# Kernel tuning notes

Measured on AMD Instinct MI355X. Metric: run time of the kernel, lower is better.

The kernel has to match this reference:

```python
import jax, jax.numpy as jnp
import numpy as np
from jax import lax

C = 512          # in_channels
L = 4            # fcos_conv_layers
NUM_CLS = 1      # fcos_num_class - 1
PRIOR_BIAS = float(-np.log((1 - 0.01) / 0.01))
BN_EPS = 1e-5


def conv1d(x, w, b, pad):
    # x: [B, Cin, T], w: [Cout, Cin, K]
    y = lax.conv_general_dilated(x, w, window_strides=(1,), padding=[(pad, pad)],
                                 dimension_numbers=('NCH', 'OIH', 'NCH'))
    return y + b[None, :, None]


def bn(x, g, b, m, v):
    inv = lax.rsqrt(v + BN_EPS)
    return (x - m[None, :, None]) * (g * inv)[None, :, None] + b[None, :, None]


def tower(x, ws, bs, gs, bes, ms, vs):
    # ws: [L, C, C, 3]; fixed small loop over layers
    for i in range(L):
        x = jax.nn.relu(bn(conv1d(x, ws[i], bs[i], 1), gs[i], bes[i], ms[i], vs[i]))
    return x


def setup_inputs() -> dict:
    key = jax.random.key(0)
    ks = jax.random.split(key, 32)
    d = {}
    d['f0'] = jax.random.normal(ks[0], (8, C, 1024), jnp.float32)
    d['f1'] = jax.random.normal(ks[1], (8, C, 512), jnp.float32)
    d['f2'] = jax.random.normal(ks[2], (8, C, 256), jnp.float32)

    def nrm(k, shape):
        return 0.01 * jax.random.normal(k, shape, jnp.float32)

    # cls / bbox towers: stacked conv + BN params
    d['cls_tw_w'] = nrm(ks[3], (L, C, C, 3)); d['cls_tw_b'] = jnp.zeros((L, C))
    d['cls_bn_g'] = jnp.ones((L, C)); d['cls_bn_b'] = jnp.zeros((L, C))
    d['cls_bn_m'] = jnp.zeros((L, C)); d['cls_bn_v'] = jnp.ones((L, C))
    d['box_tw_w'] = nrm(ks[4], (L, C, C, 3)); d['box_tw_b'] = jnp.zeros((L, C))
    d['box_bn_g'] = jnp.ones((L, C)); d['box_bn_b'] = jnp.zeros((L, C))
    d['box_bn_m'] = jnp.zeros((L, C)); d['box_bn_v'] = jnp.ones((L, C))

    d['logits_w'] = nrm(ks[5], (NUM_CLS, C, 3))
    d['logits_b'] = jnp.full((NUM_CLS,), PRIOR_BIAS, jnp.float32)
    d['bbox_w'] = nrm(ks[6], (2, C, 3)); d['bbox_b'] = jnp.zeros((2,))

    d['mix_w'] = nrm(ks[7], (C, 2 * C, 1)); d['mix_b'] = jnp.zeros((C,))
    d['mix_bn_g'] = jnp.ones((C,)); d['mix_bn_b'] = jnp.zeros((C,))
    d['mix_bn_m'] = jnp.zeros((C,)); d['mix_bn_v'] = jnp.ones((C,))

    d['iou_w1'] = nrm(ks[8], (C // 2, C, 3)); d['iou_b1'] = jnp.zeros((C // 2,))
    d['iou_bn_g'] = jnp.ones((C // 2,)); d['iou_bn_b'] = jnp.zeros((C // 2,))
    d['iou_bn_m'] = jnp.zeros((C // 2,)); d['iou_bn_v'] = jnp.ones((C // 2,))
    d['iou_w2'] = nrm(ks[9], (1, C // 2, 1)); d['iou_b2'] = jnp.zeros((1,))

    d['scales'] = jnp.ones((3,), jnp.float32)
    return d


def reference(f0, f1, f2,
              cls_tw_w, cls_tw_b, cls_bn_g, cls_bn_b, cls_bn_m, cls_bn_v,
              box_tw_w, box_tw_b, box_bn_g, box_bn_b, box_bn_m, box_bn_v,
              logits_w, logits_b, bbox_w, bbox_b,
              mix_w, mix_b, mix_bn_g, mix_bn_b, mix_bn_m, mix_bn_v,
              iou_w1, iou_b1, iou_bn_g, iou_bn_b, iou_bn_m, iou_bn_v,
              iou_w2, iou_b2, scales):
    outs = []
    for l, x in enumerate([f0, f1, f2]):
        ct = tower(x, cls_tw_w, cls_tw_b, cls_bn_g, cls_bn_b, cls_bn_m, cls_bn_v)
        bt = tower(x, box_tw_w, box_tw_b, box_bn_g, box_bn_b, box_bn_m, box_bn_v)
        logits = conv1d(ct, logits_w, logits_b, 1)                      # [B, 1, T]
        bbox = jnp.exp(conv1d(bt, bbox_w, bbox_b, 1) * scales[l])       # [B, 2, T]
        mix = jax.nn.relu(bn(conv1d(jnp.concatenate([ct, bt], axis=1), mix_w, mix_b, 0),
                             mix_bn_g, mix_bn_b, mix_bn_m, mix_bn_v))   # [B, C, T]
        h = jax.nn.relu(bn(conv1d(mix, iou_w1, iou_b1, 1),
                           iou_bn_g, iou_bn_b, iou_bn_m, iou_bn_v))
        iou = conv1d(h, iou_w2, iou_b2, 0)                              # [B, 1, T]
        outs.append(jnp.concatenate([logits, bbox, iou], axis=1))       # [B, 4, T]
    return jnp.concatenate(outs, axis=-1)  # [B, 4, T0+T1+T2]
```

## Files before the change

kernel.cpp:

```cpp
#include <hip/hip_runtime.h>
#include <hip/hip_bf16.h>


typedef __bf16 bf16x8 __attribute__((ext_vector_type(8)));
typedef float f32x4 __attribute__((ext_vector_type(4)));

__device__ __forceinline__ float bf2f(unsigned short u) {
    union { unsigned int i; float f; } c; c.i = ((unsigned int)u) << 16; return c.f;
}
__device__ __forceinline__ unsigned short f2bf(float f) {
    union { __hip_bfloat16 h; unsigned short u; } c; c.h = __float2bfloat16(f); return c.u;
}

__device__ __forceinline__ void gload16(const void* g, void* l) {
    __builtin_amdgcn_global_load_lds(
        (const __attribute__((address_space(1))) unsigned int*)g,
        (__attribute__((address_space(3))) unsigned int*)l,
        16, 0, 0);
}

__device__ __forceinline__ void tile_decode(int ct, int& rowstart, int& t0, int& Tl) {
    if (ct < 64)      { Tl = 1024; int b = ct >> 3;                 t0 = (ct & 7) << 7; rowstart = b * 1026 + 1; }
    else if (ct < 96) { Tl = 512;  int i = ct - 64; int b = i >> 2; t0 = (i & 3) << 7; rowstart = 8208 + b * 514 + 1; }
    else              { Tl = 256;  int i = ct - 96; int b = i >> 1; t0 = (i & 1) << 7; rowstart = 12320 + b * 258 + 1; }
}

__global__ __launch_bounds__(256, 2)
void conv_tower(const unsigned short* __restrict__ X, int xstride, int ci_twstride,
                const unsigned short* __restrict__ W,
                const float* __restrict__ Bs,
                unsigned short* __restrict__ Y)
{
    __shared__ alignas(16) unsigned short Xb[2][9 * 512];
    __shared__ alignas(16) unsigned short Wb[3][16 * 512];
    constexpr int XBSZ = 9 * 512;
    constexpr int WBSZ = 16 * 512;
    constexpr int XBYTES = XBSZ * 2;
    constexpr int WBYTES = WBSZ * 2;

    const int L = blockIdx.x;
    const int P = (L & 7) * 56 + (L >> 3);
    const int ct = P >> 2, sub = P & 3;
    const int tw = sub >> 1, co0 = (sub & 1) << 8;

    int rowstart, t0, Tl;
    tile_decode(ct, rowstart, t0, Tl);
    const int rtile = rowstart + t0;

    const int tid = threadIdx.x, lane = tid & 63, wid = tid >> 6;
    const int wco = (wid >> 1) << 7;
    const int wt  = (wid & 1) << 6;
    const int lr = lane & 15, sr = lane >> 4;

    const unsigned short* Wp = W + (size_t)tw * 3145728;
    const float* Bp = Bs + tw * 2048;
    const int co_out0 = tw * 512 + co0;
    const int ci_off = tw * ci_twstride;

    const unsigned short* xga[3]; unsigned short* xl[3];
#pragma unroll
    for (int p = 0; p < 3; ++p) {
        int seg = (p < 2) ? (p * 4 + wid) : 8;
        xl[p] = (unsigned short*)Xb[0] + seg * 512;
        int row = seg * 16 + (lane >> 2);
        int sc = (lane & 3) ^ ((row >> 1) & 3);
        xga[p] = X + (size_t)(rtile - 1 + row) * xstride + ci_off + sc * 8;
    }
    const unsigned short* wga[4]; unsigned short* wl[4];
#pragma unroll
    for (int p = 0; p < 4; ++p) {
        int seg = p * 4 + wid;
        wl[p] = (unsigned short*)Wb[0] + seg * 512;
        int row = seg * 16 + (lane >> 2);
        int sc = (lane & 3) ^ ((row >> 1) & 3);
        wga[p] = Wp + (size_t)(co0 + row) * 1536 + sc * 8;
    }

    int aoff[8];
#pragma unroll
    for (int mi = 0; mi < 8; ++mi) {
        int ra = wco + mi * 16 + lr;
        aoff[mi] = ra * 64 + (((sr ^ (ra >> 1)) & 3) << 4);
    }
    int boff[3][4];
#pragma unroll
    for (int kk = 0; kk < 3; ++kk)
#pragma unroll
        for (int ni = 0; ni < 4; ++ni) {
            int rb = wt + ni * 16 + lr + kk;
            boff[kk][ni] = rb * 64 + (((sr ^ (rb >> 1)) & 3) << 4);
        }

    f32x4 acc[8][4];
#pragma unroll
    for (int i = 0; i < 8; ++i)
#pragma unroll
        for (int j = 0; j < 4; ++j) acc[i][j] = (f32x4){0.f, 0.f, 0.f, 0.f};

#pragma unroll
    for (int p = 0; p < 3; ++p) gload16(xga[p], xl[p]);
#pragma unroll
    for (int p = 0; p < 4; ++p) {
        gload16(wga[p],       wl[p]);
        gload16(wga[p] + 512, wl[p] + WBSZ);
    }
    asm volatile("s_waitcnt vmcnt(0)" ::: "memory");
    __builtin_amdgcn_s_barrier();

#pragma unroll
    for (int s = 0; s < 48; ++s) {
        const int kk = s % 3, k0 = s / 3;
        if      (s == 47) asm volatile("s_waitcnt vmcnt(0)" ::: "memory");
        else if (s == 46) asm volatile("s_waitcnt vmcnt(4)" ::: "memory");
        else if (kk == 0) asm volatile("s_waitcnt vmcnt(4)" ::: "memory");
        else              asm volatile("s_waitcnt vmcnt(7)" ::: "memory");
        __builtin_amdgcn_s_barrier();

        if (s + 2 <= 47) {
            const int u = s + 2, ut = u % 3, uk = u / 3;
#pragma unroll
            for (int p = 0; p < 4; ++p)
                gload16(wga[p] + ut * 512 + uk * 32, wl[p] + ut * WBSZ);
        }
        if (kk == 0 && k0 + 1 <= 15) {
#pragma unroll
            for (int p = 0; p < 3; ++p)
                gload16(xga[p] + (k0 + 1) * 32, xl[p] + ((k0 + 1) & 1) * XBSZ);
        }

        const char* wbuf = (const char*)Wb[0] + (s % 3) * WBYTES;
        const char* xbuf = (const char*)Xb[0] + (k0 & 1) * XBYTES;
        bf16x8 af[8], bv[4];
#pragma unroll
        for (int mi = 0; mi < 8; ++mi)
            af[mi] = *(const bf16x8*)(wbuf + aoff[mi]);
#pragma unroll
        for (int ni = 0; ni < 4; ++ni)
            bv[ni] = *(const bf16x8*)(xbuf + boff[kk][ni]);
        __builtin_amdgcn_s_setprio(1);
#pragma unroll
        for (int mi = 0; mi < 8; ++mi)
#pragma unroll
            for (int ni = 0; ni < 4; ++ni)
                acc[mi][ni] = __builtin_amdgcn_mfma_f32_16x16x32_bf16(af[mi], bv[ni], acc[mi][ni], 0, 0, 0);
        __builtin_amdgcn_s_setprio(0);
        __builtin_amdgcn_s_barrier();
    }

    const int r4 = sr * 4;
#pragma unroll
    for (int mi = 0; mi < 8; ++mi) {
        int co_l = wco + mi * 16 + r4;
        float b0 = Bp[co0 + co_l + 0], b1 = Bp[co0 + co_l + 1];
        float b2 = Bp[co0 + co_l + 2], b3 = Bp[co0 + co_l + 3];
#pragma unroll
        for (int ni = 0; ni < 4; ++ni) {
            int t = wt + ni * 16 + lr;
            f32x4 a = acc[mi][ni];
            float v0 = fmaxf(a[0] + b0, 0.f), v1 = fmaxf(a[1] + b1, 0.f);
            float v2 = fmaxf(a[2] + b2, 0.f), v3 = fmaxf(a[3] + b3, 0.f);
            union { unsigned long long u; unsigned short s[4]; } pk2;
            pk2.s[0] = f2bf(v0); pk2.s[1] = f2bf(v1); pk2.s[2] = f2bf(v2); pk2.s[3] = f2bf(v3);
            *(unsigned long long*)(Y + (size_t)(rtile + t) * 1024 + co_out0 + co_l) = pk2.u;
        }
    }
}

template<int KSIZE>
__global__ __launch_bounds__(256)
void conv_gemm(const unsigned short* __restrict__ X, int xstride, int ci0_base, int ci_twstride, int Cin,
               const unsigned short* __restrict__ W, int w_twstride,
               const float* __restrict__ Bs, int b_twstride,
               unsigned short* __restrict__ Y, int ystride, int co_twstride,
               int relu)
{
    constexpr int BM = 128, BN = 128, BK = 32;
    constexpr int NR = BN + KSIZE - 1;
    constexpr int XSEG = (NR * 64 + 1023) / 1024;
    constexpr int XPW  = (XSEG + 3) / 4;
    constexpr int WSEG = KSIZE * BM * 64 / 1024;
    constexpr int WPW  = WSEG / 4;
    __shared__ alignas(16) unsigned short Xs[2 * XSEG * 512];
    __shared__ alignas(16) unsigned short Ws[2 * WSEG * 512];

    const int tid = threadIdx.x;
    const int lane = tid & 63, wid = tid >> 6;
    int rowstart, t0, Tl;
    tile_decode(blockIdx.x, rowstart, t0, Tl);
    const int co0 = blockIdx.y * BM;
    const int tw = blockIdx.z;
    const int ci_off = ci0_base + tw * ci_twstride;
    const unsigned short* Wp = W + (size_t)tw * w_twstride;
    const float* Bp = Bs + tw * b_twstride;
    const int co_out0 = tw * co_twstride + co0;

    const int wm = (wid >> 1) * 64, wn = (wid & 1) * 64;
    const int lr = lane & 15;
    const int sr = lane >> 4;

    const unsigned short* xga[XPW]; unsigned short* xl[XPW];
#pragma unroll
    for (int p = 0; p < XPW; ++p) {
        int seg = (KSIZE == 3) ? ((p < 2) ? p * 4 + wid : 8) : (p * 4 + wid);
        xl[p] = Xs + seg * 512;
        int g = seg * 64 + lane;
        int row = g >> 2, s = (g & 3) ^ ((row >> 1) & 3);
        xga[p] = X + (size_t)(rowstart + t0 - (KSIZE >> 1) + row) * xstride + ci_off + s * 8;
    }
    const unsigned short* wga[WPW]; unsigned short* wl[WPW];
#pragma unroll
    for (int p = 0; p < WPW; ++p) {
        int seg = p * 4 + wid;
        wl[p] = Ws + seg * 512;
        int g = seg * 64 + lane;
        int row = g >> 2, s = (g & 3) ^ ((row >> 1) & 3);
        int co = row & (BM - 1), kk = row >> 7;
        wga[p] = Wp + (size_t)(co0 + co) * (KSIZE * Cin) + kk * Cin + s * 8;
    }

    f32x4 acc[4][4];
#pragma unroll
    for (int i = 0; i < 4; ++i)
#pragma unroll
        for (int j = 0; j < 4; ++j) acc[i][j] = (f32x4){0.f, 0.f, 0.f, 0.f};

    auto STAGE = [&](int buf) {
#pragma unroll
        for (int p = 0; p < XPW; ++p) { gload16(xga[p], xl[p] + buf * (XSEG * 512)); xga[p] += BK; }
#pragma unroll
        for (int p = 0; p < WPW; ++p) { gload16(wga[p], wl[p] + buf * (WSEG * 512)); wga[p] += BK; }
    };

    const int nk = Cin / BK;
    STAGE(0);
    int cur = 0;
    for (int ks = 0; ks < nk; ++ks) {
        if (ks + 1 < nk) {
            STAGE(cur ^ 1);
            if constexpr (KSIZE == 3) asm volatile("s_waitcnt vmcnt(9)" ::: "memory");
            else                      asm volatile("s_waitcnt vmcnt(4)" ::: "memory");
        } else {
            asm volatile("s_waitcnt vmcnt(0)" ::: "memory");
        }
        __builtin_amdgcn_sched_barrier(0);
        __builtin_amdgcn_s_barrier();

        const char* bXs = (const char*)Xs + cur * (XSEG * 1024);
        const char* bWs = (const char*)Ws + cur * (WSEG * 1024);
#pragma unroll
        for (int kk = 0; kk < KSIZE; ++kk) {
            bf16x8 af[4], bv[4];
#pragma unroll
            for (int mi = 0; mi < 4; ++mi) {
                int ra = kk * BM + wm + mi * 16 + lr;
                af[mi] = *(const bf16x8*)(bWs + ra * 64 + (((sr ^ (ra >> 1)) & 3) << 4));
                int rb = wn + mi * 16 + lr + kk;
                bv[mi] = *(const bf16x8*)(bXs + rb * 64 + (((sr ^ (rb >> 1)) & 3) << 4));
            }
#pragma unroll
            for (int mi = 0; mi < 4; ++mi)
#pragma unroll
                for (int ni = 0; ni < 4; ++ni)
                    acc[mi][ni] = __builtin_amdgcn_mfma_f32_16x16x32_bf16(af[mi], bv[ni], acc[mi][ni], 0, 0, 0);
        }
        __builtin_amdgcn_sched_barrier(0);
        __builtin_amdgcn_s_barrier();
        cur ^= 1;
    }

    const int r4 = (lane >> 4) * 4;
#pragma unroll
    for (int mi = 0; mi < 4; ++mi) {
        int co_l = wm + mi * 16 + r4;
        float b0 = Bp[co0 + co_l + 0], b1 = Bp[co0 + co_l + 1];
        float b2 = Bp[co0 + co_l + 2], b3 = Bp[co0 + co_l + 3];
#pragma unroll
        for (int ni = 0; ni < 4; ++ni) {
            int t = t0 + wn + ni * 16 + lr;
            f32x4 a = acc[mi][ni];
            float v0 = a[0] + b0, v1 = a[1] + b1, v2 = a[2] + b2, v3 = a[3] + b3;
            if (relu) {
                v0 = fmaxf(v0, 0.f); v1 = fmaxf(v1, 0.f);
                v2 = fmaxf(v2, 0.f); v3 = fmaxf(v3, 0.f);
            }
            union { unsigned long long u; unsigned short s[4]; } pk;
            pk.s[0] = f2bf(v0); pk.s[1] = f2bf(v1); pk.s[2] = f2bf(v2); pk.s[3] = f2bf(v3);
            *(unsigned long long*)(Y + (size_t)(rowstart + t) * ystride + co_out0 + co_l) = pk.u;
        }
    }
}

__global__ __launch_bounds__(256)
void zero_pads(unsigned short* __restrict__ act0, unsigned short* __restrict__ catA,
               unsigned short* __restrict__ catB, unsigned short* __restrict__ mixo,
               unsigned short* __restrict__ iouh)
{
    int c = blockIdx.x >> 1, side = blockIdx.x & 1;
    int start, Tl;
    if (c < 8)       { start = c * 1026;               Tl = 1024; }
    else if (c < 16) { start = 8208 + (c - 8) * 514;   Tl = 512;  }
    else             { start = 12320 + (c - 16) * 258; Tl = 256;  }
    size_t prow = start + (side ? Tl + 1 : 0);
    int tid = threadIdx.x;
    uint4 z = make_uint4(0u, 0u, 0u, 0u);
    if (tid < 64)  *(uint4*)(act0 + prow * 512 + tid * 8) = z;
    if (tid < 128) { *(uint4*)(catA + prow * 1024 + tid * 8) = z;
                     *(uint4*)(catB + prow * 1024 + tid * 8) = z; }
    if (tid >= 128 && tid < 192) *(uint4*)(mixo + prow * 512 + (tid - 128) * 8) = z;
    if (tid >= 192 && tid < 224) *(uint4*)(iouh + prow * 256 + (tid - 192) * 8) = z;
}

__global__ __launch_bounds__(256)
void transpose_in(const float* __restrict__ f0, const float* __restrict__ f1, const float* __restrict__ f2,
                  unsigned short* __restrict__ act0)
{
    __shared__ float tile[32][33];
    int bx = blockIdx.x;
    const float* src; int Tl, padbase, b, t0;
    if (bx < 256)      { src = f0; Tl = 1024; int i = bx;       b = i >> 5; t0 = (i & 31) << 5; padbase = b * 1026; }
    else if (bx < 384) { src = f1; Tl = 512;  int i = bx - 256; b = i >> 4; t0 = (i & 15) << 5; padbase = 8208 + b * 514; }
    else               { src = f2; Tl = 256;  int i = bx - 384; b = i >> 3; t0 = (i & 7)  << 5; padbase = 12320 + b * 258; }
    int c0 = blockIdx.y << 5;
    const float* sb = src + (size_t)b * 512 * Tl;
    int tl = threadIdx.x & 31, cl = threadIdx.x >> 5;
#pragma unroll
    for (int j = 0; j < 4; ++j) {
        int c = cl + j * 8;
        tile[c][tl] = sb[(size_t)(c0 + c) * Tl + t0 + tl];
    }
    __syncthreads();
    int cc = threadIdx.x & 31, tr0 = threadIdx.x >> 5;
    size_t base = (size_t)(padbase + 1 + t0) * 512 + c0;
#pragma unroll
    for (int j = 0; j < 4; ++j) {
        int tr = tr0 + j * 8;
        act0[base + (size_t)tr * 512 + cc] = f2bf(tile[cc][tr]);
    }
}

__global__ __launch_bounds__(256)
void prep_tower(const float* __restrict__ cls_w, const float* __restrict__ box_w,
                const float* __restrict__ cg, const float* __restrict__ cvv,
                const float* __restrict__ bg, const float* __restrict__ bvv,
                unsigned short* __restrict__ Wt)
{
    int idx = blockIdx.x * 256 + threadIdx.x;
    if (idx >= 2 * 4 * 512 * 3 * 512) return;
    int ci = idx & 511;
    int kk = (idx >> 9) % 3;
    int co = (idx / 1536) & 511;
    int l  = (idx / 786432) & 3;
    int tw = idx / 3145728;
    const float* w = tw ? box_w : cls_w;
    const float* g = tw ? bg : cg;
    const float* v = tw ? bvv : cvv;
    float s = g[l * 512 + co] * rsqrtf(v[l * 512 + co] + 1e-5f);
    float val = w[(((size_t)(l * 512 + co)) * 512 + ci) * 3 + kk] * s;
    Wt[idx] = f2bf(val);
}

__global__ __launch_bounds__(256)
void prep_misc(const float* mix_w, const float* mix_b, const float* mg, const float* mbeta, const float* mm, const float* mv,
               const float* iou_w1, const float* iou_b1, const float* ig, const float* ibeta, const float* im, const float* iv,
               const float* cls_b, const float* cg, const float* cbeta, const float* cm, const float* cv2,
               const float* box_b, const float* bg, const float* bbeta, const float* bm, const float* bv2,
               unsigned short* Wmix, unsigned short* Wiou, float* Bt, float* Bmix, float* Biou)
{
    int idx = blockIdx.x * 256 + threadIdx.x;
    if (idx < 524288) {
        int co = idx >> 10;
        float s = mg[co] * rsqrtf(mv[co] + 1e-5f);
        Wmix[idx] = f2bf(mix_w[idx] * s);
        return;
    }
    idx -= 524288;
    if (idx < 393216) {
        int ci = idx & 511, kk = (idx >> 9) % 3, co = idx / 1536;
        float s = ig[co] * rsqrtf(iv[co] + 1e-5f);
        Wiou[idx] = f2bf(iou_w1[((size_t)(co * 512 + ci)) * 3 + kk] * s);
        return;
    }
    idx -= 393216;
    if (idx < 4096) {
        int co = idx & 511, l = (idx >> 9) & 3, tw = idx >> 11;
        const float* g = tw ? bg : cg; const float* v = tw ? bv2 : cv2;
        const float* m = tw ? bm : cm; const float* be = tw ? bbeta : cbeta;
        const float* cb = tw ? box_b : cls_b;
        int o = l * 512 + co;
        float s = g[o] * rsqrtf(v[o] + 1e-5f);
        Bt[idx] = (cb[o] - m[o]) * s + be[o];
        return;
    }
    idx -= 4096;
    if (idx < 512) {
        float s = mg[idx] * rsqrtf(mv[idx] + 1e-5f);
        Bmix[idx] = (mix_b[idx] - mm[idx]) * s + mbeta[idx];
        return;
    }
    idx -= 512;
    if (idx < 256) {
        float s = ig[idx] * rsqrtf(iv[idx] + 1e-5f);
        Biou[idx] = (iou_b1[idx] - im[idx]) * s + ibeta[idx];
    }
}

__global__ __launch_bounds__(256)
void heads_kernel(const unsigned short* __restrict__ catb, const unsigned short* __restrict__ iouh,
                  const float* __restrict__ lw, const float* __restrict__ lb,
                  const float* __restrict__ bw, const float* __restrict__ bb,
                  const float* __restrict__ iw, const float* __restrict__ ib,
                  const float* __restrict__ scales, float* __restrict__ out)
{
    const int lane = threadIdx.x & 63;
    const int wid = threadIdx.x >> 6;

    float lwr[24], bwr0[24], bwr1[24], iwr[4];
    {
        const float4* p = (const float4*)(lw + lane * 24);
#pragma unroll
        for (int q = 0; q < 6; ++q) {
            float4 v = p[q];
            lwr[q * 4 + 0] = v.x; lwr[q * 4 + 1] = v.y; lwr[q * 4 + 2] = v.z; lwr[q * 4 + 3] = v.w;
        }
        p = (const float4*)(bw + lane * 24);
#pragma unroll
        for (int q = 0; q < 6; ++q) {
            float4 v = p[q];
            bwr0[q * 4 + 0] = v.x; bwr0[q * 4 + 1] = v.y; bwr0[q * 4 + 2] = v.z; bwr0[q * 4 + 3] = v.w;
        }
        p = (const float4*)(bw + 1536 + lane * 24);
#pragma unroll
        for (int q = 0; q < 6; ++q) {
            float4 v = p[q];
            bwr1[q * 4 + 0] = v.x; bwr1[q * 4 + 1] = v.y; bwr1[q * 4 + 2] = v.z; bwr1[q * 4 + 3] = v.w;
        }
        float4 v = *(const float4*)(iw + lane * 4);
        iwr[0] = v.x; iwr[1] = v.y; iwr[2] = v.z; iwr[3] = v.w;
    }
    const float lb0 = lb[0], bb0 = bb[0], bb1 = bb[1], ib0 = ib[0];
    const float s0 = scales[0], s1 = scales[1], s2 = scales[2];

    for (int r = blockIdx.x * 4 + wid; r < 14336; r += gridDim.x * 4) {
        int tlog, roff, tgoff, padbase; float sc;
        if (r < 8192)       { tlog = 10; roff = 0;     tgoff = 0;    sc = s0; }
        else if (r < 12288) { tlog = 9;  roff = 8192;  tgoff = 1024; sc = s1; }
        else                { tlog = 8;  roff = 12288; tgoff = 1536; sc = s2; }
        int i = r - roff;
        int Tl = 1 << tlog;
        int b = i >> tlog, t = i & (Tl - 1);
        if (r < 8192)       padbase = b * 1026;
        else if (r < 12288) padbase = 8208 + b * 514;
        else                padbase = 12320 + b * 258;
        int prow = padbase + 1 + t;

        float al = 0.f, a0 = 0.f, a1 = 0.f, ai = 0.f;
        const unsigned short* base = catb + (size_t)prow * 1024 + lane * 8;
#pragma unroll
        for (int kk = 0; kk < 3; ++kk) {
            union { uint4 u; unsigned short s[8]; } cv, bvv;
            cv.u = *(const uint4*)(base + (kk - 1) * 1024);
            bvv.u = *(const uint4*)(base + (kk - 1) * 1024 + 512);
#pragma unroll
            for (int j = 0; j < 8; ++j) {
                float xc = bf2f(cv.s[j]);
                float xb = bf2f(bvv.s[j]);
                al = fmaf(xc, lwr[j * 3 + kk], al);
                a0 = fmaf(xb, bwr0[j * 3 + kk], a0);
                a1 = fmaf(xb, bwr1[j * 3 + kk], a1);
            }
        }
        {
            union { uint2 u; unsigned short s[4]; } hv;
            hv.u = *(const uint2*)(iouh + (size_t)prow * 256 + lane * 4);
#pragma unroll
            for (int j = 0; j < 4; ++j) ai = fmaf(bf2f(hv.s[j]), iwr[j], ai);
        }
#pragma unroll
        for (int off = 32; off > 0; off >>= 1) {
            al += __shfl_xor(al, off);
            a0 += __shfl_xor(a0, off);
            a1 += __shfl_xor(a1, off);
            ai += __shfl_xor(ai, off);
        }
        if (lane == 0) {
            int tg = tgoff + t;
            out[((size_t)b * 4 + 0) * 1792 + tg] = al + lb0;
            out[((size_t)b * 4 + 1) * 1792 + tg] = expf((a0 + bb0) * sc);
            out[((size_t)b * 4 + 2) * 1792 + tg] = expf((a1 + bb1) * sc);
            out[((size_t)b * 4 + 3) * 1792 + tg] = ai + ib0;
        }
    }
}

extern "C" void kernel_launch(void* const* d_in, const int* in_sizes, int n_in,
                              void* d_out, int out_size, void* d_ws, size_t ws_size,
                              hipStream_t stream)
{
    const float* f0       = (const float*)d_in[0];
    const float* f1       = (const float*)d_in[1];
    const float* f2       = (const float*)d_in[2];
    const float* cls_tw_w = (const float*)d_in[3];
    const float* cls_tw_b = (const float*)d_in[4];
    const float* cls_bn_g = (const float*)d_in[5];
    const float* cls_bn_b = (const float*)d_in[6];
    const float* cls_bn_m = (const float*)d_in[7];
    const float* cls_bn_v = (const float*)d_in[8];
    const float* box_tw_w = (const float*)d_in[9];
    const float* box_tw_b = (const float*)d_in[10];
    const float* box_bn_g = (const float*)d_in[11];
    const float* box_bn_b = (const float*)d_in[12];
    const float* box_bn_m = (const float*)d_in[13];
    const float* box_bn_v = (const float*)d_in[14];
    const float* logits_w = (const float*)d_in[15];
    const float* logits_b = (const float*)d_in[16];
    const float* bbox_w   = (const float*)d_in[17];
    const float* bbox_b   = (const float*)d_in[18];
    const float* mix_w    = (const float*)d_in[19];
    const float* mix_b    = (const float*)d_in[20];
    const float* mix_bn_g = (const float*)d_in[21];
    const float* mix_bn_b = (const float*)d_in[22];
    const float* mix_bn_m = (const float*)d_in[23];
    const float* mix_bn_v = (const float*)d_in[24];
    const float* iou_w1   = (const float*)d_in[25];
    const float* iou_b1   = (const float*)d_in[26];
    const float* iou_bn_g = (const float*)d_in[27];
    const float* iou_bn_b = (const float*)d_in[28];
    const float* iou_bn_m = (const float*)d_in[29];
    const float* iou_bn_v = (const float*)d_in[30];
    const float* iou_w2   = (const float*)d_in[31];
    const float* iou_b2   = (const float*)d_in[32];
    const float* scales   = (const float*)d_in[33];

    unsigned char* ws = (unsigned char*)d_ws;
    unsigned short* Wt   = (unsigned short*)(ws + 0);
    unsigned short* Wmix = (unsigned short*)(ws + 12582912);
    unsigned short* Wiou = (unsigned short*)(ws + 13631488);
    float*          Bt   = (float*)(ws + 14417920);
    float*          Bmix = (float*)(ws + 14434304);
    float*          Biou = (float*)(ws + 14436352);
    unsigned short* act0 = (unsigned short*)(ws + 14437376);
    unsigned short* catA = (unsigned short*)(ws + 29182976);
    unsigned short* catB = (unsigned short*)(ws + 58674176);
    unsigned short* mixo = (unsigned short*)(ws + 88165376);
    unsigned short* iouh = (unsigned short*)(ws + 102910976);

    zero_pads<<<dim3(48), dim3(256), 0, stream>>>(act0, catA, catB, mixo, iouh);
    prep_tower<<<dim3(24576), dim3(256), 0, stream>>>(cls_tw_w, box_tw_w, cls_bn_g, cls_bn_v,
                                                      box_bn_g, box_bn_v, Wt);
    prep_misc<<<dim3(3603), dim3(256), 0, stream>>>(mix_w, mix_b, mix_bn_g, mix_bn_b, mix_bn_m, mix_bn_v,
                                                    iou_w1, iou_b1, iou_bn_g, iou_bn_b, iou_bn_m, iou_bn_v,
                                                    cls_tw_b, cls_bn_g, cls_bn_b, cls_bn_m, cls_bn_v,
                                                    box_tw_b, box_bn_g, box_bn_b, box_bn_m, box_bn_v,
                                                    Wmix, Wiou, Bt, Bmix, Biou);
    transpose_in<<<dim3(448, 16), dim3(256), 0, stream>>>(f0, f1, f2, act0);

    conv_tower<<<dim3(448), dim3(256), 0, stream>>>(act0, 512, 0,    Wt,            Bt,        catA);
    conv_tower<<<dim3(448), dim3(256), 0, stream>>>(catA, 1024, 512, Wt + 786432,  Bt + 512,  catB);
    conv_tower<<<dim3(448), dim3(256), 0, stream>>>(catB, 1024, 512, Wt + 1572864, Bt + 1024, catA);
    conv_tower<<<dim3(448), dim3(256), 0, stream>>>(catA, 1024, 512, Wt + 2359296, Bt + 1536, catB);
    conv_gemm<1><<<dim3(112, 4, 1), 256, 0, stream>>>(catB, 1024, 0, 0, 1024,
                                                      Wmix, 0, Bmix, 0, mixo, 512, 0, 1);
    conv_gemm<3><<<dim3(112, 2, 1), 256, 0, stream>>>(mixo, 512, 0, 0, 512,
                                                      Wiou, 0, Biou, 0, iouh, 256, 0, 1);
    heads_kernel<<<dim3(896), dim3(256), 0, stream>>>(catB, iouh, logits_w, logits_b,
                                                      bbox_w, bbox_b, iou_w2, iou_b2, scales,
                                                      (float*)d_out);
}
```

Measured before the change: 297.9 us.

## Enlarge conv_tower tiles to 256 time steps with 8-wave blocks and split-phase pipeline

Each conv_tower block now covers 256 time rows with 512 threads (8 waves), so it launches half as many blocks (224 instead of 448) and each weight tile is reused across twice as many time steps. The main loop is split into two half-steps per k-slice, interleaving global-to-LDS loads, LDS fragment reads and MFMAs, with retuned vmcnt waits and an explicit lgkmcnt wait. The aim is to cut weight traffic and LDS pressure per output. In exchange occupancy drops to one block per CU, there are fewer blocks than the 256 CUs, and barriers per step double. sched_barriers are also removed from conv_gemm.

Result: slower. 317.0 us (+6.4%).

```diff
diff --git a/kernel.cpp b/kernel.cpp
--- a/kernel.cpp
+++ b/kernel.cpp
@@ -25,31 +25,32 @@
     else              { Tl = 256;  int i = ct - 96; int b = i >> 1; t0 = (i & 1) << 7; rowstart = 12320 + b * 258 + 1; }
 }
 
-__global__ __launch_bounds__(256, 2)
+__global__ __launch_bounds__(512, 1)
 void conv_tower(const unsigned short* __restrict__ X, int xstride, int ci_twstride,
                 const unsigned short* __restrict__ W,
                 const float* __restrict__ Bs,
                 unsigned short* __restrict__ Y)
 {
-    __shared__ alignas(16) unsigned short Xb[2][9 * 512];
+    __shared__ alignas(16) unsigned short Xb[2][17 * 512];
     __shared__ alignas(16) unsigned short Wb[3][16 * 512];
-    constexpr int XBSZ = 9 * 512;
+    constexpr int XBSZ = 17 * 512;
     constexpr int WBSZ = 16 * 512;
     constexpr int XBYTES = XBSZ * 2;
     constexpr int WBYTES = WBSZ * 2;
 
     const int L = blockIdx.x;
-    const int P = (L & 7) * 56 + (L >> 3);
-    const int ct = P >> 2, sub = P & 3;
+    const int P = (L & 7) * 28 + (L >> 3);
+    const int tt = P >> 2, sub = P & 3;
     const int tw = sub >> 1, co0 = (sub & 1) << 8;
 
-    int rowstart, t0, Tl;
-    tile_decode(ct, rowstart, t0, Tl);
-    const int rtile = rowstart + t0;
+    int rowstart;
+    if (tt < 32)      { rowstart = (tt >> 2) * 1026 + 1 + ((tt & 3) << 8); }
+    else if (tt < 48) { int i = tt - 32; rowstart = 8208 + (i >> 1) * 514 + 1 + ((i & 1) << 8); }
+    else              { rowstart = 12320 + (tt - 48) * 258 + 1; }
 
     const int tid = threadIdx.x, lane = tid & 63, wid = tid >> 6;
-    const int wco = (wid >> 1) << 7;
-    const int wt  = (wid & 1) << 6;
+    const int wco = (wid >> 2) << 7;
+    const int wt  = (wid & 3) << 6;
     const int lr = lane & 15, sr = lane >> 4;
 
     const unsigned short* Wp = W + (size_t)tw * 3145728;
@@ -60,28 +61,30 @@
     const unsigned short* xga[3]; unsigned short* xl[3];
 #pragma unroll
     for (int p = 0; p < 3; ++p) {
-        int seg = (p < 2) ? (p * 4 + wid) : 8;
+        int seg = (p < 2) ? (p * 8 + wid) : 16;
         xl[p] = (unsigned short*)Xb[0] + seg * 512;
         int row = seg * 16 + (lane >> 2);
         int sc = (lane & 3) ^ ((row >> 1) & 3);
-        xga[p] = X + (size_t)(rtile - 1 + row) * xstride + ci_off + sc * 8;
-    }
-    const unsigned short* wga[4]; unsigned short* wl[4];
-#pragma unroll
-    for (int p = 0; p < 4; ++p) {
-        int seg = p * 4 + wid;
+        xga[p] = X + (size_t)(rowstart - 1 + row) * xstride + ci_off + sc * 8;
+    }
+    const unsigned short* wga[2]; unsigned short* wl[2];
+#pragma unroll
+    for (int p = 0; p < 2; ++p) {
+        int seg = p * 8 + wid;
         wl[p] = (unsigned short*)Wb[0] + seg * 512;
         int row = seg * 16 + (lane >> 2);
         int sc = (lane & 3) ^ ((row >> 1) & 3);
         wga[p] = Wp + (size_t)(co0 + row) * 1536 + sc * 8;
     }
 
-    int aoff[8];
-#pragma unroll
-    for (int mi = 0; mi < 8; ++mi) {
-        int ra = wco + mi * 16 + lr;
-        aoff[mi] = ra * 64 + (((sr ^ (ra >> 1)) & 3) << 4);
-    }
+    int aoff[2][4];
+#pragma unroll
+    for (int h = 0; h < 2; ++h)
+#pragma unroll
+        for (int mi = 0; mi < 4; ++mi) {
+            int ra = wco + h * 64 + mi * 16 + lr;
+            aoff[h][mi] = ra * 64 + (((sr ^ (ra >> 1)) & 3) << 4);
+        }
     int boff[3][4];
 #pragma unroll
     for (int kk = 0; kk < 3; ++kk)
@@ -100,68 +103,79 @@
 #pragma unroll
     for (int p = 0; p < 3; ++p) gload16(xga[p], xl[p]);
 #pragma unroll
-    for (int p = 0; p < 4; ++p) {
+    for (int p = 0; p < 2; ++p) {
         gload16(wga[p],       wl[p]);
         gload16(wga[p] + 512, wl[p] + WBSZ);
     }
     asm volatile("s_waitcnt vmcnt(0)" ::: "memory");
     __builtin_amdgcn_s_barrier();
 
-#pragma unroll
-    for (int s = 0; s < 48; ++s) {
+    bf16x8 bv[4];
+#pragma unroll
+    for (int q = 0; q < 96; ++q) {
+        const int s = q >> 1, h = q & 1;
         const int kk = s % 3, k0 = s / 3;
-        if      (s == 47) asm volatile("s_waitcnt vmcnt(0)" ::: "memory");
-        else if (s == 46) asm volatile("s_waitcnt vmcnt(4)" ::: "memory");
-        else if (kk == 0) asm volatile("s_waitcnt vmcnt(4)" ::: "memory");
-        else              asm volatile("s_waitcnt vmcnt(7)" ::: "memory");
-        __builtin_amdgcn_s_barrier();
-
-        if (s + 2 <= 47) {
-            const int u = s + 2, ut = u % 3, uk = u / 3;
-#pragma unroll
-            for (int p = 0; p < 4; ++p)
-                gload16(wga[p] + ut * 512 + uk * 32, wl[p] + ut * WBSZ);
-        }
-        if (kk == 0 && k0 + 1 <= 15) {
-#pragma unroll
-            for (int p = 0; p < 3; ++p)
-                gload16(xga[p] + (k0 + 1) * 32, xl[p] + ((k0 + 1) & 1) * XBSZ);
+
+        if (h == 0 && s > 0) {
+            if      (s == 47) asm volatile("s_waitcnt vmcnt(0)" ::: "memory");
+            else if (s == 46) asm volatile("s_waitcnt vmcnt(2)" ::: "memory");
+            else if (kk == 0) asm volatile("s_waitcnt vmcnt(2)" ::: "memory");
+            else if (kk == 1) asm volatile("s_waitcnt vmcnt(4)" ::: "memory");
+            else              asm volatile("s_waitcnt vmcnt(3)" ::: "memory");
         }
 
         const char* wbuf = (const char*)Wb[0] + (s % 3) * WBYTES;
         const char* xbuf = (const char*)Xb[0] + (k0 & 1) * XBYTES;
-        bf16x8 af[8], bv[4];
-#pragma unroll
-        for (int mi = 0; mi < 8; ++mi)
-            af[mi] = *(const bf16x8*)(wbuf + aoff[mi]);
-#pragma unroll
-        for (int ni = 0; ni < 4; ++ni)
-            bv[ni] = *(const bf16x8*)(xbuf + boff[kk][ni]);
+        bf16x8 af[4];
+#pragma unroll
+        for (int mi = 0; mi < 4; ++mi)
+            af[mi] = *(const bf16x8*)(wbuf + aoff[h][mi]);
+        if (h == 0) {
+#pragma unroll
+            for (int ni = 0; ni < 4; ++ni)
+                bv[ni] = *(const bf16x8*)(xbuf + boff[kk][ni]);
+        }
+
+        if (s + 2 <= 47) {
+            const int u = s + 2;
+            gload16(wga[h] + (u % 3) * 512 + (u / 3) * 32, wl[h] + (u % 3) * WBSZ);
+        }
+        if (k0 <= 14) {
+            if (kk == 0)
+                gload16(xga[h] + (k0 + 1) * 32, xl[h] + ((k0 + 1) & 1) * XBSZ);
+            else if (kk == 1 && h == 0)
+                gload16(xga[2] + (k0 + 1) * 32, xl[2] + ((k0 + 1) & 1) * XBSZ);
+        }
+
+        __builtin_amdgcn_s_barrier();
+        asm volatile("s_waitcnt lgkmcnt(0)" ::: "memory");
+        __builtin_amdgcn_sched_barrier(0);
         __builtin_amdgcn_s_setprio(1);
 #pragma unroll
-        for (int mi = 0; mi < 8; ++mi)
+        for (int mi = 0; mi < 4; ++mi)
 #pragma unroll
             for (int ni = 0; ni < 4; ++ni)
-                acc[mi][ni] = __builtin_amdgcn_mfma_f32_16x16x32_bf16(af[mi], bv[ni], acc[mi][ni], 0, 0, 0);
+                acc[h * 4 + mi][ni] = __builtin_amdgcn_mfma_f32_16x16x32_bf16(af[mi], bv[ni], acc[h * 4 + mi][ni], 0, 0, 0);
         __builtin_amdgcn_s_setprio(0);
+        __builtin_amdgcn_sched_barrier(0);
         __builtin_amdgcn_s_barrier();
     }
 
     const int r4 = sr * 4;
 #pragma unroll
-    for (int mi = 0; mi < 8; ++mi) {
-        int co_l = wco + mi * 16 + r4;
+    for (int hm = 0; hm < 8; ++hm) {
+        int co_l = wco + hm * 16 + r4;
         float b0 = Bp[co0 + co_l + 0], b1 = Bp[co0 + co_l + 1];
         float b2 = Bp[co0 + co_l + 2], b3 = Bp[co0 + co_l + 3];
 #pragma unroll
         for (int ni = 0; ni < 4; ++ni) {
             int t = wt + ni * 16 + lr;
-            f32x4 a = acc[mi][ni];
+            f32x4 a = acc[hm][ni];
             float v0 = fmaxf(a[0] + b0, 0.f), v1 = fmaxf(a[1] + b1, 0.f);
             float v2 = fmaxf(a[2] + b2, 0.f), v3 = fmaxf(a[3] + b3, 0.f);
             union { unsigned long long u; unsigned short s[4]; } pk2;
             pk2.s[0] = f2bf(v0); pk2.s[1] = f2bf(v1); pk2.s[2] = f2bf(v2); pk2.s[3] = f2bf(v3);
-            *(unsigned long long*)(Y + (size_t)(rtile + t) * 1024 + co_out0 + co_l) = pk2.u;
+            *(unsigned long long*)(Y + (size_t)(rowstart + t) * 1024 + co_out0 + co_l) = pk2.u;
         }
     }
 }
@@ -242,7 +256,6 @@
         } else {
             asm volatile("s_waitcnt vmcnt(0)" ::: "memory");
         }
-        __builtin_amdgcn_sched_barrier(0);
         __builtin_amdgcn_s_barrier();
 
         const char* bXs = (const char*)Xs + cur * (XSEG * 1024);
@@ -263,7 +276,6 @@
                 for (int ni = 0; ni < 4; ++ni)
                     acc[mi][ni] = __builtin_amdgcn_mfma_f32_16x16x32_bf16(af[mi], bv[ni], acc[mi][ni], 0, 0, 0);
         }
-        __builtin_amdgcn_sched_barrier(0);
         __builtin_amdgcn_s_barrier();
         cur ^= 1;
     }
@@ -554,10 +566,10 @@
                                                     Wmix, Wiou, Bt, Bmix, Biou);
     transpose_in<<<dim3(448, 16), dim3(256), 0, stream>>>(f0, f1, f2, act0);
 
-    conv_tower<<<dim3(448), dim3(256), 0, stream>>>(act0, 512, 0,    Wt,            Bt,        catA);
-    conv_tower<<<dim3(448), dim3(256), 0, stream>>>(catA, 1024, 512, Wt + 786432,  Bt + 512,  catB);
-    conv_tower<<<dim3(448), dim3(256), 0, stream>>>(catB, 1024, 512, Wt + 1572864, Bt + 1024, catA);
-    conv_tower<<<dim3(448), dim3(256), 0, stream>>>(catA, 1024, 512, Wt + 2359296, Bt + 1536, catB);
+    conv_tower<<<dim3(224), dim3(512), 0, stream>>>(act0, 512, 0,    Wt,            Bt,        catA);
+    conv_tower<<<dim3(224), dim3(512), 0, stream>>>(catA, 1024, 512, Wt + 786432,  Bt + 512,  catB);
+    conv_tower<<<dim3(224), dim3(512), 0, stream>>>(catB, 1024, 512, Wt + 1572864, Bt + 1024, catA);
+    conv_tower<<<dim3(224), dim3(512), 0, stream>>>(catA, 1024, 512, Wt + 2359296, Bt + 1536, catB);
     conv_gemm<1><<<dim3(112, 4, 1), 256, 0, stream>>>(catB, 1024, 0, 0, 1024,
                                                       Wmix, 0, Bmix, 0, mixo, 512, 0, 1);
     conv_gemm<3><<<dim3(112, 2, 1), 256, 0, stream>>>(mixo, 512, 0, 0, 512,
```
